# Optimization experiments

Hardware: AMD Instinct MI355X
Metric: run time of the kernel (lower is better)

## Reference

```python
import jax, jax.numpy as jnp
import numpy as np

N_NODES = 50000
N_EDGES = 400000


def setup_inputs() -> dict:
    key = jax.random.key(0)
    k1, k2, k3, k4 = jax.random.split(key, 4)
    in_feat = jax.random.normal(k1, (2, 64, 4, N_NODES), dtype=jnp.float32)
    src = jax.random.randint(k2, (N_EDGES,), 0, N_NODES, dtype=jnp.int32)
    dst = jax.random.randint(k3, (N_EDGES,), 0, N_NODES, dtype=jnp.int32)
    W = jax.random.normal(k4, (64, 64), dtype=jnp.float32) * (1.0 / 8.0)
    b = jnp.zeros((64,), dtype=jnp.float32)
    return {"in_feat": in_feat, "src": src, "dst": dst, "W": W, "b": b}


def reference(in_feat, src, dst, W, b):
    # in_feat: (B, h, T, N). Net permutation [3,1,2,0] then [0,3,2,1] == [3,0,2,1]
    x = jnp.transpose(in_feat, (3, 0, 2, 1))  # (N, B, T, h) -- node-major for GraphConv
    N = x.shape[0]
    ones_e = jnp.ones(src.shape[0], dtype=x.dtype)
    deg_out = jnp.clip(jax.ops.segment_sum(ones_e, src, num_segments=N), 1.0)
    deg_in = jnp.clip(jax.ops.segment_sum(ones_e, dst, num_segments=N), 1.0)
    # DGL GraphConv, norm='both', in_feats == out_feats -> aggregate then matmul
    x = x * jax.lax.rsqrt(deg_out)[:, None, None, None]
    agg = jax.ops.segment_sum(x[src], dst, num_segments=N)  # (N, B, T, h)
    agg = agg * jax.lax.rsqrt(deg_in)[:, None, None, None]
    h = jnp.einsum('nbth,hf->nbtf', agg, W) + b
    h = jax.nn.relu(h)
    # inverse permutation [0,3,2,1] then [3,1,2,0] == transpose(h, (1,3,2,0))
    out = jnp.transpose(h, (1, 3, 2, 0))  # (B, h, T, N)
    return jax.nn.relu(out)
```

## Files before the change

### kernel.cpp

```cpp
#include <hip/hip_runtime.h>
#include <hip/hip_fp16.h>


extern "C" __global__ void k_zero(int* __restrict__ p, int n) {
  int i = blockIdx.x * blockDim.x + threadIdx.x;
  if (i < n) p[i] = 0;
}

extern "C" __global__ void k_deg(const int* __restrict__ src, const int* __restrict__ dst,
                                 int* __restrict__ deg_out, int* __restrict__ deg_in, int E) {
  int e = blockIdx.x * blockDim.x + threadIdx.x;
  if (e < E) {
    atomicAdd(&deg_out[src[e]], 1);
    atomicAdd(&deg_in[dst[e]], 1);
  }
}

extern "C" __global__ void k_rsqrt(const int* __restrict__ dgo, const int* __restrict__ dgi,
                                   float* __restrict__ rs_out, float* __restrict__ rs_in, int N) {
  int i = blockIdx.x * blockDim.x + threadIdx.x;
  if (i < N) {
    int a = dgo[i] > 1 ? dgo[i] : 1;
    int b = dgi[i] > 1 ? dgi[i] : 1;
    rs_out[i] = rsqrtf((float)a);
    rs_in[i]  = rsqrtf((float)b);
  }
}

extern "C" __global__ __launch_bounds__(256) void k_scan1(const int* __restrict__ deg,
                                                          int* __restrict__ bsum, int N) {
  __shared__ int red[256];
  int tid = threadIdx.x;
  int i = blockIdx.x * 256 + tid;
  red[tid] = (i < N) ? deg[i] : 0;
  __syncthreads();
  #pragma unroll
  for (int off = 128; off > 0; off >>= 1) {
    if (tid < off) red[tid] += red[tid + off];
    __syncthreads();
  }
  if (tid == 0) bsum[blockIdx.x] = red[0];
}

extern "C" __global__ __launch_bounds__(256) void k_scan2(const int* __restrict__ bsum,
                                                          int* __restrict__ boffs,
                                                          int* __restrict__ offs, int M, int N) {
  __shared__ int sc[256];
  int tid = threadIdx.x;
  int v = (tid < M) ? bsum[tid] : 0;
  sc[tid] = v;
  __syncthreads();
  #pragma unroll
  for (int off = 1; off < 256; off <<= 1) {
    int t = sc[tid];
    if (tid >= off) t += sc[tid - off];
    __syncthreads();
    sc[tid] = t;
    __syncthreads();
  }
  boffs[tid] = sc[tid] - v;
  if (tid == 255) offs[N] = sc[255];
}

extern "C" __global__ __launch_bounds__(256) void k_scan3(const int* __restrict__ deg,
                                                          const int* __restrict__ boffs,
                                                          int* __restrict__ offs, int N) {
  __shared__ int sc[256];
  int tid = threadIdx.x;
  int i = blockIdx.x * 256 + tid;
  int v = (i < N) ? deg[i] : 0;
  sc[tid] = v;
  __syncthreads();
  #pragma unroll
  for (int off = 1; off < 256; off <<= 1) {
    int t = sc[tid];
    if (tid >= off) t += sc[tid - off];
    __syncthreads();
    sc[tid] = t;
    __syncthreads();
  }
  if (i < N) offs[i] = boffs[blockIdx.x] + sc[tid] - v;
}

extern "C" __global__ void k_scatter(const int* __restrict__ src, const int* __restrict__ dst,
                                     const int* __restrict__ offs, int* __restrict__ cursor,
                                     int* __restrict__ csr_src, int E) {
  int e = blockIdx.x * blockDim.x + threadIdx.x;
  if (e < E) {
    int d = dst[e];
    int pos = offs[d] + atomicAdd(&cursor[d], 1);
    csr_src[pos] = src[e];
  }
}

extern "C" __global__ __launch_bounds__(256) void k_transform(
    const float* __restrict__ in_feat, const float* __restrict__ W,
    const float* __restrict__ rs_out, __half* __restrict__ y, int N) {
  int tid = threadIdx.x;
  int wave = tid >> 6, lane = tid & 63;
  int bt = blockIdx.y * 4 + wave;
  int b = bt >> 2, t = bt & 3;
  int fh = blockIdx.z * 32;
  int n = blockIdx.x * 64 + lane;

  const float* xp = in_feat + (size_t)(b * 256 + t) * (size_t)N;
  size_t hstride = (size_t)4 * (size_t)N;

  float acc[32];
  #pragma unroll
  for (int f = 0; f < 32; ++f) acc[f] = 0.0f;

  bool ok = (n < N);

  float xcur[4], xnxt[4];
  #pragma unroll
  for (int u = 0; u < 4; ++u)
    xcur[u] = ok ? xp[(size_t)u * hstride + n] : 0.0f;

  #pragma unroll 1
  for (int h0 = 0; h0 < 60; h0 += 4) {
    #pragma unroll
    for (int u = 0; u < 4; ++u)
      xnxt[u] = ok ? xp[(size_t)(h0 + 4 + u) * hstride + n] : 0.0f;
    #pragma unroll
    for (int u = 0; u < 4; ++u) {
      const float* wrow = W + (h0 + u) * 64 + fh;
      #pragma unroll
      for (int f = 0; f < 32; ++f) acc[f] = fmaf(xcur[u], wrow[f], acc[f]);
    }
    #pragma unroll
    for (int u = 0; u < 4; ++u) xcur[u] = xnxt[u];
  }
  #pragma unroll
  for (int u = 0; u < 4; ++u) {
    const float* wrow = W + (60 + u) * 64 + fh;
    #pragma unroll
    for (int f = 0; f < 32; ++f) acc[f] = fmaf(xcur[u], wrow[f], acc[f]);
  }

  if (ok) {
    float rs = rs_out[n];
    union { unsigned int u[16]; uint4 v[4]; } pk;
    #pragma unroll
    for (int q = 0; q < 16; ++q) {
      __half2 h2 = __float22half2_rn(make_float2(acc[2 * q] * rs, acc[2 * q + 1] * rs));
      pk.u[q] = *(unsigned int*)&h2;
    }
    uint4* yp = (uint4*)(y + (size_t)n * 512 + bt * 64 + fh);
    #pragma unroll
    for (int q = 0; q < 4; ++q) yp[q] = pk.v[q];
  }
}

extern "C" __global__ __launch_bounds__(512) void k_aggregate(
    const __half* __restrict__ y, const int* __restrict__ offs,
    const int* __restrict__ csr_src, const float* __restrict__ rs_in,
    const float* __restrict__ bvec, float* __restrict__ out, int N) {
  __shared__ float agg[16 * 513];
  int tid = threadIdx.x;
  int lane = tid & 63, wave = tid >> 6;
  int n0 = blockIdx.x * 16;

#define ACC_EDGE(s)                                                          \
  {                                                                          \
    const uint2* rp = (const uint2*)(y + (size_t)(s) * 512);                 \
    uint2 ua = rp[lane];                                                     \
    uint2 ub = rp[64 + lane];                                                \
    float2 f;                                                                \
    f = __half22float2(*(const __half2*)&ua.x); accA.x += f.x; accA.y += f.y;\
    f = __half22float2(*(const __half2*)&ua.y); accA.z += f.x; accA.w += f.y;\
    f = __half22float2(*(const __half2*)&ub.x); accB.x += f.x; accB.y += f.y;\
    f = __half22float2(*(const __half2*)&ub.y); accB.z += f.x; accB.w += f.y;\
  }

  #pragma unroll
  for (int k = 0; k < 2; ++k) {
    int nl = k * 8 + wave;
    int n = n0 + nl;
    float4 accA = {0.f, 0.f, 0.f, 0.f};
    float4 accB = {0.f, 0.f, 0.f, 0.f};
    if (n < N) {
      int j0 = offs[n], j1 = offs[n + 1];
      for (int base = j0; base < j1; base += 64) {
        int idxv = csr_src[base + lane];
        int m = j1 - base; if (m > 64) m = 64;
        int e = 0;
        for (; e + 3 < m; e += 4) {
          int s0 = __builtin_amdgcn_readlane(idxv, e);
          int s1 = __builtin_amdgcn_readlane(idxv, e + 1);
          int s2 = __builtin_amdgcn_readlane(idxv, e + 2);
          int s3 = __builtin_amdgcn_readlane(idxv, e + 3);
          ACC_EDGE(s0); ACC_EDGE(s1); ACC_EDGE(s2); ACC_EDGE(s3);
        }
        for (; e < m; ++e) {
          int s0 = __builtin_amdgcn_readlane(idxv, e);
          ACC_EDGE(s0);
        }
      }
    }
    *(float4*)&agg[nl * 513 + lane * 4] = accA;
    *(float4*)&agg[nl * 513 + 256 + lane * 4] = accB;
  }
#undef ACC_EDGE
  __syncthreads();

  int nl = tid & 15;
  int r0 = tid >> 4;
  int n = n0 + nl;
  float rs = (n < N) ? rs_in[n] : 0.0f;
  #pragma unroll 4
  for (int it = 0; it < 16; ++it) {
    int c = it * 32 + r0;
    float v = agg[nl * 513 + c];
    int f = c & 63, bt = c >> 6;
    int b = bt >> 2, t = bt & 3;
    v = v * rs + bvec[f];
    v = fmaxf(v, 0.0f);
    if (n < N) out[(size_t)((b * 64 + f) * 4 + t) * (size_t)N + n] = v;
  }
}

extern "C" void kernel_launch(void* const* d_in, const int* in_sizes, int n_in,
                              void* d_out, int out_size, void* d_ws, size_t ws_size,
                              hipStream_t stream) {
  const float* in_feat = (const float*)d_in[0];
  const int*   src     = (const int*)d_in[1];
  const int*   dst     = (const int*)d_in[2];
  const float* W       = (const float*)d_in[3];
  const float* bvec    = (const float*)d_in[4];
  float* out = (float*)d_out;

  int N = in_sizes[0] / 512;
  int E = in_sizes[1];

  int A  = (N + 64) & ~63;
  int EA = (E + 63) & ~63;
  int M  = (N + 255) / 256;

  int*   deg_out_i = (int*)d_ws;
  int*   deg_in_i  = deg_out_i + A;
  int*   cursor    = deg_in_i + A;
  int*   offs      = cursor + A;
  int*   bsum      = offs + A;
  int*   boffs     = bsum + 256;
  float* rs_out    = (float*)(boffs + 256);
  float* rs_in     = rs_out + A;
  int*   csr_src   = (int*)(rs_in + A);
  __half* y        = (__half*)(csr_src + EA);

  int z = 3 * A;
  hipLaunchKernelGGL(k_zero, dim3((z + 255) / 256), dim3(256), 0, stream, deg_out_i, z);
  hipLaunchKernelGGL(k_deg, dim3((E + 255) / 256), dim3(256), 0, stream,
                     src, dst, deg_out_i, deg_in_i, E);
  hipLaunchKernelGGL(k_rsqrt, dim3((N + 255) / 256), dim3(256), 0, stream,
                     deg_out_i, deg_in_i, rs_out, rs_in, N);
  hipLaunchKernelGGL(k_scan1, dim3(M), dim3(256), 0, stream, deg_in_i, bsum, N);
  hipLaunchKernelGGL(k_scan2, dim3(1), dim3(256), 0, stream, bsum, boffs, offs, M, N);
  hipLaunchKernelGGL(k_scan3, dim3(M), dim3(256), 0, stream, deg_in_i, boffs, offs, N);
  hipLaunchKernelGGL(k_scatter, dim3((E + 255) / 256), dim3(256), 0, stream,
                     src, dst, offs, cursor, csr_src, E);
  hipLaunchKernelGGL(k_transform, dim3((N + 63) / 64, 2, 2), dim3(256), 0, stream,
                     in_feat, W, rs_out, y, N);
  hipLaunchKernelGGL(k_aggregate, dim3((N + 15) / 16), dim3(512), 0, stream,
                     y, offs, csr_src, rs_in, bvec, out, N);
}
```

Before: 197.0 us.

## Fuse rsqrt into scan, memset instead of zero kernel, full-width transform per thread

Folds the degree rsqrt computation into the first scan kernel and replaces the zeroing kernel with hipMemsetAsync, dropping two launches. The transform kernel now computes all 64 output features per thread instead of splitting them across two z-blocks, so each input feature is read once rather than twice. In exchange each thread holds 64 accumulators, which raises register pressure (launch bounds set to 2 blocks per CU) and may lower occupancy.

```diff
diff --git a/kernel.cpp b/kernel.cpp
--- a/kernel.cpp
+++ b/kernel.cpp
@@ -1,11 +1,6 @@
 #include <hip/hip_runtime.h>
 #include <hip/hip_fp16.h>
 
-
-extern "C" __global__ void k_zero(int* __restrict__ p, int n) {
-  int i = blockIdx.x * blockDim.x + threadIdx.x;
-  if (i < n) p[i] = 0;
-}
 
 extern "C" __global__ void k_deg(const int* __restrict__ src, const int* __restrict__ dst,
                                  int* __restrict__ deg_out, int* __restrict__ deg_in, int E) {
@@ -16,23 +11,22 @@
   }
 }
 
-extern "C" __global__ void k_rsqrt(const int* __restrict__ dgo, const int* __restrict__ dgi,
-                                   float* __restrict__ rs_out, float* __restrict__ rs_in, int N) {
-  int i = blockIdx.x * blockDim.x + threadIdx.x;
+extern "C" __global__ __launch_bounds__(256) void k_scan1(const int* __restrict__ deg_in,
+                                                          const int* __restrict__ deg_out,
+                                                          int* __restrict__ bsum,
+                                                          float* __restrict__ rs_out,
+                                                          float* __restrict__ rs_in, int N) {
+  __shared__ int red[256];
+  int tid = threadIdx.x;
+  int i = blockIdx.x * 256 + tid;
+  int di = (i < N) ? deg_in[i] : 0;
+  red[tid] = di;
   if (i < N) {
-    int a = dgo[i] > 1 ? dgo[i] : 1;
-    int b = dgi[i] > 1 ? dgi[i] : 1;
+    int a = deg_out[i] > 1 ? deg_out[i] : 1;
+    int b = di > 1 ? di : 1;
     rs_out[i] = rsqrtf((float)a);
     rs_in[i]  = rsqrtf((float)b);
   }
-}
-
-extern "C" __global__ __launch_bounds__(256) void k_scan1(const int* __restrict__ deg,
-                                                          int* __restrict__ bsum, int N) {
-  __shared__ int red[256];
-  int tid = threadIdx.x;
-  int i = blockIdx.x * 256 + tid;
-  red[tid] = (i < N) ? deg[i] : 0;
   __syncthreads();
   #pragma unroll
   for (int off = 128; off > 0; off >>= 1) {
@@ -93,22 +87,21 @@
   }
 }
 
-extern "C" __global__ __launch_bounds__(256) void k_transform(
+extern "C" __global__ __launch_bounds__(256, 2) void k_transform(
     const float* __restrict__ in_feat, const float* __restrict__ W,
     const float* __restrict__ rs_out, __half* __restrict__ y, int N) {
   int tid = threadIdx.x;
   int wave = tid >> 6, lane = tid & 63;
   int bt = blockIdx.y * 4 + wave;
   int b = bt >> 2, t = bt & 3;
-  int fh = blockIdx.z * 32;
   int n = blockIdx.x * 64 + lane;
 
   const float* xp = in_feat + (size_t)(b * 256 + t) * (size_t)N;
   size_t hstride = (size_t)4 * (size_t)N;
 
-  float acc[32];
-  #pragma unroll
-  for (int f = 0; f < 32; ++f) acc[f] = 0.0f;
+  float acc[64];
+  #pragma unroll
+  for (int f = 0; f < 64; ++f) acc[f] = 0.0f;
 
   bool ok = (n < N);
 
@@ -124,31 +117,31 @@
       xnxt[u] = ok ? xp[(size_t)(h0 + 4 + u) * hstride + n] : 0.0f;
     #pragma unroll
     for (int u = 0; u < 4; ++u) {
-      const float* wrow = W + (h0 + u) * 64 + fh;
+      const float* wrow = W + (h0 + u) * 64;
       #pragma unroll
-      for (int f = 0; f < 32; ++f) acc[f] = fmaf(xcur[u], wrow[f], acc[f]);
+      for (int f = 0; f < 64; ++f) acc[f] = fmaf(xcur[u], wrow[f], acc[f]);
     }
     #pragma unroll
     for (int u = 0; u < 4; ++u) xcur[u] = xnxt[u];
   }
   #pragma unroll
   for (int u = 0; u < 4; ++u) {
-    const float* wrow = W + (60 + u) * 64 + fh;
-    #pragma unroll
-    for (int f = 0; f < 32; ++f) acc[f] = fmaf(xcur[u], wrow[f], acc[f]);
+    const float* wrow = W + (60 + u) * 64;
+    #pragma unroll
+    for (int f = 0; f < 64; ++f) acc[f] = fmaf(xcur[u], wrow[f], acc[f]);
   }
 
   if (ok) {
     float rs = rs_out[n];
-    union { unsigned int u[16]; uint4 v[4]; } pk;
-    #pragma unroll
-    for (int q = 0; q < 16; ++q) {
+    union { unsigned int u[32]; uint4 v[8]; } pk;
+    #pragma unroll
+    for (int q = 0; q < 32; ++q) {
       __half2 h2 = __float22half2_rn(make_float2(acc[2 * q] * rs, acc[2 * q + 1] * rs));
       pk.u[q] = *(unsigned int*)&h2;
     }
-    uint4* yp = (uint4*)(y + (size_t)n * 512 + bt * 64 + fh);
-    #pragma unroll
-    for (int q = 0; q < 4; ++q) yp[q] = pk.v[q];
+    uint4* yp = (uint4*)(y + (size_t)n * 512 + bt * 64);
+    #pragma unroll
+    for (int q = 0; q < 8; ++q) yp[q] = pk.v[q];
   }
 }
 
@@ -248,18 +241,16 @@
   int*   csr_src   = (int*)(rs_in + A);
   __half* y        = (__half*)(csr_src + EA);
 
-  int z = 3 * A;
-  hipLaunchKernelGGL(k_zero, dim3((z + 255) / 256), dim3(256), 0, stream, deg_out_i, z);
+  hipMemsetAsync(deg_out_i, 0, (size_t)(3 * A) * sizeof(int), stream);
   hipLaunchKernelGGL(k_deg, dim3((E + 255) / 256), dim3(256), 0, stream,
                      src, dst, deg_out_i, deg_in_i, E);
-  hipLaunchKernelGGL(k_rsqrt, dim3((N + 255) / 256), dim3(256), 0, stream,
-                     deg_out_i, deg_in_i, rs_out, rs_in, N);
-  hipLaunchKernelGGL(k_scan1, dim3(M), dim3(256), 0, stream, deg_in_i, bsum, N);
+  hipLaunchKernelGGL(k_scan1, dim3(M), dim3(256), 0, stream,
+                     deg_in_i, deg_out_i, bsum, rs_out, rs_in, N);
   hipLaunchKernelGGL(k_scan2, dim3(1), dim3(256), 0, stream, bsum, boffs, offs, M, N);
   hipLaunchKernelGGL(k_scan3, dim3(M), dim3(256), 0, stream, deg_in_i, boffs, offs, N);
   hipLaunchKernelGGL(k_scatter, dim3((E + 255) / 256), dim3(256), 0, stream,
                      src, dst, offs, cursor, csr_src, E);
-  hipLaunchKernelGGL(k_transform, dim3((N + 63) / 64, 2, 2), dim3(256), 0, stream,
+  hipLaunchKernelGGL(k_transform, dim3((N + 63) / 64, 2, 1), dim3(256), 0, stream,
                      in_feat, W, rs_out, y, N);
   hipLaunchKernelGGL(k_aggregate, dim3((N + 15) / 16), dim3(512), 0, stream,
                      y, offs, csr_src, rs_in, bvec, out, N);
```

After: 206.0 us. +4.6%, slower.
